# Kernel optimization log

Measured on AMD Instinct MI355X. Metric: run time of the kernel, lower is better.

The kernel has to match this reference:

```python
import jax, jax.numpy as jnp
import numpy as np
import math

N_EMBD = 1024
N_HEAD = 16
D_FF = 4 * N_EMBD
B, T = 4, 2048

def gelu_tanh(x):
    return 0.5 * x * (1.0 + jnp.tanh(jnp.sqrt(2.0 / jnp.pi).astype(x.dtype) * (x + 0.044715 * x ** 3)))

def layernorm(x, g, b, eps=1e-5):
    mu = jnp.mean(x, axis=-1, keepdims=True)
    var = jnp.var(x, axis=-1, keepdims=True)
    return (x - mu) * jax.lax.rsqrt(var + eps) * g + b

def setup_inputs() -> dict:
    key = jax.random.key(0)
    ks = jax.random.split(key, 12)
    s = lambda fan_in: 1.0 / np.sqrt(fan_in)
    return {
        "x": jax.random.normal(ks[0], (B, T, N_EMBD), jnp.float32),
        "ln1_g": jnp.ones((N_EMBD,), jnp.float32),
        "ln1_b": jnp.zeros((N_EMBD,), jnp.float32),
        "w_attn": jax.random.normal(ks[1], (N_EMBD, 3 * N_EMBD), jnp.float32) * s(N_EMBD),
        "b_attn": jnp.zeros((3 * N_EMBD,), jnp.float32),
        "w_proj": jax.random.normal(ks[2], (N_EMBD, N_EMBD), jnp.float32) * s(N_EMBD),
        "b_proj": jnp.zeros((N_EMBD,), jnp.float32),
        "ln2_g": jnp.ones((N_EMBD,), jnp.float32),
        "ln2_b": jnp.zeros((N_EMBD,), jnp.float32),
        "w_fc": jax.random.normal(ks[3], (N_EMBD, D_FF), jnp.float32) * s(N_EMBD),
        "b_fc": jnp.zeros((D_FF,), jnp.float32),
        "w_fc2": jax.random.normal(ks[4], (D_FF, N_EMBD), jnp.float32) * s(D_FF),
        "b_fc2": jnp.zeros((N_EMBD,), jnp.float32),
    }

def reference(x, ln1_g, ln1_b, w_attn, b_attn, w_proj, b_proj,
              ln2_g, ln2_b, w_fc, b_fc, w_fc2, b_fc2):
    Bn, Tn, C = x.shape
    hs = C // N_HEAD
    # --- attention ---
    h = layernorm(x, ln1_g, ln1_b)
    qkv = h @ w_attn + b_attn  # [B,T,3C]
    q, k, v = jnp.split(qkv, 3, axis=-1)
    q = q.reshape(Bn, Tn, N_HEAD, hs).transpose(0, 2, 1, 3)
    k = k.reshape(Bn, Tn, N_HEAD, hs).transpose(0, 2, 1, 3)
    v = v.reshape(Bn, Tn, N_HEAD, hs).transpose(0, 2, 1, 3)
    att = jnp.einsum('bhqd,bhkd->bhqk', q, k) * (hs ** -0.5)
    mask = jnp.tril(jnp.ones((Tn, Tn), bool))
    att = jnp.where(mask, att, -jnp.inf)
    att = jax.nn.softmax(att, axis=-1)
    y = jnp.einsum('bhqk,bhkd->bhqd', att, v)
    y = y.transpose(0, 2, 1, 3).reshape(Bn, Tn, C)
    x = x + (y @ w_proj + b_proj)
    # --- MLP ---
    h2 = layernorm(x, ln2_g, ln2_b)
    h2 = gelu_tanh(h2 @ w_fc + b_fc)
    x = x + (h2 @ w_fc2 + b_fc2)
    return x
```

## Files before the change

### kernel.cpp

```cpp
#include <hip/hip_runtime.h>
#include <hip/hip_bf16.h>

#define B_ 4
#define T_ 2048
#define C_ 1024
#define NH_ 16
#define FF_ 4096
#define NT_ (B_*T_)

typedef short bf16x8 __attribute__((ext_vector_type(8)));
typedef float f32x4 __attribute__((ext_vector_type(4)));

#define LDS_AS(p) ((__attribute__((address_space(3))) uint32_t*)(p))
#define GLB_AS(p) ((const __attribute__((address_space(1))) uint32_t*)(p))

__device__ __forceinline__ float bf2f(__hip_bfloat16 v){ return __bfloat162float(v); }
__device__ __forceinline__ __hip_bfloat16 f2bf(float f){ return __float2bfloat16(f); }

__device__ __forceinline__ f32x4 mfma16(bf16x8 a, bf16x8 b, f32x4 c){
  return __builtin_amdgcn_mfma_f32_16x16x32_bf16(a, b, c, 0, 0, 0);
}

__global__ __launch_bounds__(256) void transpose_bf16(const float* __restrict__ in,
                                                      __hip_bfloat16* __restrict__ out,
                                                      int K, int N) {
  __shared__ float tile[32][33];
  const int n0 = blockIdx.x * 32, k0 = blockIdx.y * 32;
  const int x = threadIdx.x & 31, y = threadIdx.x >> 5;
  #pragma unroll
  for (int i = 0; i < 4; i++)
    tile[y + 8*i][x] = in[(size_t)(k0 + y + 8*i) * N + n0 + x];
  __syncthreads();
  #pragma unroll
  for (int i = 0; i < 4; i++)
    out[(size_t)(n0 + y + 8*i) * K + k0 + x] = f2bf(tile[x][y + 8*i]);
}

__global__ __launch_bounds__(256) void ln_bf16(const float* __restrict__ x,
                                               const float* __restrict__ g,
                                               const float* __restrict__ b,
                                               __hip_bfloat16* __restrict__ out) {
  const int row = blockIdx.x;
  const int tid = threadIdx.x;
  float4 v = ((const float4*)(x + (size_t)row * C_))[tid];
  float s  = v.x + v.y + v.z + v.w;
  float s2 = v.x*v.x + v.y*v.y + v.z*v.z + v.w*v.w;
  #pragma unroll
  for (int off = 32; off > 0; off >>= 1) {
    s  += __shfl_down(s,  off, 64);
    s2 += __shfl_down(s2, off, 64);
  }
  __shared__ float red[8];
  const int w = tid >> 6, l = tid & 63;
  if (l == 0) { red[w] = s; red[4 + w] = s2; }
  __syncthreads();
  s  = red[0] + red[1] + red[2] + red[3];
  s2 = red[4] + red[5] + red[6] + red[7];
  const float mu   = s * (1.0f / C_);
  const float var  = s2 * (1.0f / C_) - mu * mu;
  const float rstd = rsqrtf(var + 1e-5f);
  float4 gv = ((const float4*)g)[tid];
  float4 bv = ((const float4*)b)[tid];
  ushort4 o;
  __hip_bfloat16 t;
  t = f2bf((v.x - mu) * rstd * gv.x + bv.x); o.x = *(unsigned short*)&t;
  t = f2bf((v.y - mu) * rstd * gv.y + bv.y); o.y = *(unsigned short*)&t;
  t = f2bf((v.z - mu) * rstd * gv.z + bv.z); o.z = *(unsigned short*)&t;
  t = f2bf((v.w - mu) * rstd * gv.w + bv.w); o.w = *(unsigned short*)&t;
  ((ushort4*)out)[(size_t)row * (C_/4) + tid] = o;
}

template <int MODE>
__global__ __launch_bounds__(256) void gemm_bt(const __hip_bfloat16* __restrict__ A,
                                               const __hip_bfloat16* __restrict__ BT,
                                               const float* __restrict__ bias,
                                               const float* __restrict__ resid,
                                               void* __restrict__ outp,
                                               void* __restrict__ outp2,
                                               int N, int K) {
  __shared__ __hip_bfloat16 Als[128 * 64];
  __shared__ __hip_bfloat16 Bls[128 * 64];
  const int tid = threadIdx.x;
  const int w = tid >> 6, l = tid & 63;
  const int tile_n = blockIdx.x * 128;
  const int tile_m = blockIdx.y * 128;
  const int wm = (w >> 1) * 64, wn = (w & 1) * 64;

  f32x4 acc[4][4] = {};

  const int lrow8 = l >> 3;
  const int gchunk = (l & 7) ^ lrow8;
  const int m_ = (l & 15);
  const int q_ = (l >> 4);

  for (int k0 = 0; k0 < K; k0 += 64) {
    #pragma unroll
    for (int jj = 0; jj < 2; jj++) {
      const int r0 = w*16 + 8*jj + lrow8;
      __builtin_amdgcn_global_load_lds(GLB_AS(A  + (size_t)(tile_m + r0) * K + k0 + gchunk*8),
                                       LDS_AS(&Als[(w*16 + 8*jj) * 64]), 16, 0, 0);
      __builtin_amdgcn_global_load_lds(GLB_AS(A  + (size_t)(tile_m + 64 + r0) * K + k0 + gchunk*8),
                                       LDS_AS(&Als[(64 + w*16 + 8*jj) * 64]), 16, 0, 0);
      __builtin_amdgcn_global_load_lds(GLB_AS(BT + (size_t)(tile_n + r0) * K + k0 + gchunk*8),
                                       LDS_AS(&Bls[(w*16 + 8*jj) * 64]), 16, 0, 0);
      __builtin_amdgcn_global_load_lds(GLB_AS(BT + (size_t)(tile_n + 64 + r0) * K + k0 + gchunk*8),
                                       LDS_AS(&Bls[(64 + w*16 + 8*jj) * 64]), 16, 0, 0);
    }
    __syncthreads();
    bf16x8 af[2][4], bfr[2][4];
    #pragma unroll
    for (int c = 0; c < 2; c++) {
      #pragma unroll
      for (int mi = 0; mi < 4; mi++) {
        const int row = wm + mi*16 + m_;
        af[c][mi] = *(const bf16x8*)&Als[row * 64 + (((c*4 + q_) ^ (row & 7)) * 8)];
      }
      #pragma unroll
      for (int ni = 0; ni < 4; ni++) {
        const int row = wn + ni*16 + m_;
        bfr[c][ni] = *(const bf16x8*)&Bls[row * 64 + (((c*4 + q_) ^ (row & 7)) * 8)];
      }
    }
    #pragma unroll
    for (int c = 0; c < 2; c++)
      #pragma unroll
      for (int mi = 0; mi < 4; mi++)
        #pragma unroll
        for (int ni = 0; ni < 4; ni++)
          acc[mi][ni] = mfma16(af[c][mi], bfr[c][ni], acc[mi][ni]);
    __syncthreads();
  }

  const int r0 = tile_m + wm + q_ * 4;
  const int c0 = tile_n + wn + m_;
  #pragma unroll
  for (int mi = 0; mi < 4; mi++) {
    #pragma unroll
    for (int r = 0; r < 4; r++) {
      const int row = r0 + mi * 16 + r;
      #pragma unroll
      for (int ni = 0; ni < 4; ni++) {
        const int col = c0 + ni * 16;
        float v = acc[mi][ni][r] + bias[col];
        if (MODE == 0) {
          if (tile_n < 2 * C_) {
            ((__hip_bfloat16*)outp)[(size_t)row * (2*C_) + col] = f2bf(v);
          } else {
            const int dg = col - 2 * C_;
            ((__hip_bfloat16*)outp2)[((size_t)((row >> 11) * 1024 + dg)) * T_ + (row & 2047)] = f2bf(v);
          }
        } else if (MODE == 1 || MODE == 3) {
          ((float*)outp)[(size_t)row * N + col] = resid[(size_t)row * N + col] + v;
        } else {
          const float u = 0.7978845608028654f * (v + 0.044715f * v * v * v);
          const float e = __expf(2.0f * u);
          ((__hip_bfloat16*)outp)[(size_t)row * N + col] = f2bf(v * (1.0f - 1.0f / (e + 1.0f)));
        }
      }
    }
  }
}

__global__ __launch_bounds__(256, 2) void flash_attn(const __hip_bfloat16* __restrict__ qk,
                                                     const __hip_bfloat16* __restrict__ vT,
                                                     __hip_bfloat16* __restrict__ y) {
  const int id  = blockIdx.x;
  const int xcd = id & 7;
  const int jj  = id >> 3;
  const int bh  = xcd * 8 + (jj >> 3);
  const int p   = jj & 7;
  const int b   = bh >> 4, h = bh & 15;
  const int tid = threadIdx.x, w = tid >> 6, l = tid & 63;
  const int m_ = l & 15, q_ = l >> 4;

  __shared__ __hip_bfloat16 Pls[128 * 76];

  const size_t kgbase = (size_t)b * T_ * (2*C_) + C_ + h*64;
  const size_t vgbase = (size_t)bh * 64 * T_;

#define LOAD_KV(bkX, bvX, kt_) do {                                                   \
    _Pragma("unroll")                                                                 \
    for (int ni = 0; ni < 4; ni++) {                                                  \
      const __hip_bfloat16* kp = qk + kgbase + (size_t)((kt_)*64 + ni*16 + m_)*(2*C_);\
      union { uint4 u; bf16x8 f; } t0, t1;                                            \
      t0.u = *(const uint4*)(kp + q_*8);                                              \
      t1.u = *(const uint4*)(kp + 32 + q_*8);                                         \
      bkX[ni][0] = t0.f; bkX[ni][1] = t1.f;                                           \
    }                                                                                 \
    _Pragma("unroll")                                                                 \
    for (int ni = 0; ni < 4; ni++) {                                                  \
      const __hip_bfloat16* vp = vT + vgbase + (size_t)(ni*16 + m_)*T_ + (kt_)*64;    \
      union { uint4 u; bf16x8 f; } t2, t3;                                            \
      t2.u = *(const uint4*)(vp + q_*8);                                              \
      t3.u = *(const uint4*)(vp + 32 + q_*8);                                         \
      bvX[ni][0] = t2.f; bvX[ni][1] = t3.f;                                           \
    }                                                                                 \
  } while (0)

#define COMPUTE(bkX, bvX, kt_) do {                                                   \
    f32x4 s[2][4];                                                                    \
    _Pragma("unroll")                                                                 \
    for (int ni = 0; ni < 4; ni++)                                                    \
      _Pragma("unroll")                                                               \
      for (int mf = 0; mf < 2; mf++) {                                                \
        f32x4 z = {};                                                                 \
        z = mfma16(aq[mf][0], bkX[ni][0], z);                                         \
        s[mf][ni] = mfma16(aq[mf][1], bkX[ni][1], z);                                 \
      }                                                                               \
    if ((kt_) >= 2*qt) {                                                              \
      _Pragma("unroll")                                                               \
      for (int mf = 0; mf < 2; mf++) {                                                \
        const int qrow = q0 + w*32 + mf*16 + q_*4;                                    \
        _Pragma("unroll")                                                             \
        for (int ni = 0; ni < 4; ni++) {                                              \
          const int kcol = (kt_)*64 + ni*16 + m_;                                     \
          _Pragma("unroll")                                                           \
          for (int r = 0; r < 4; r++)                                                 \
            if (kcol > qrow + r) s[mf][ni][r] = -1e30f;                               \
        }                                                                             \
      }                                                                               \
    }                                                                                 \
    _Pragma("unroll")                                                                 \
    for (int mf = 0; mf < 2; mf++) {                                                  \
      _Pragma("unroll")                                                               \
      for (int ni = 0; ni < 4; ni++)                                                  \
        _Pragma("unroll")                                                             \
        for (int r = 0; r < 4; r++)                                                   \
          s[mf][ni][r] = exp2f(s[mf][ni][r]);                                         \
      _Pragma("unroll")                                                               \
      for (int r = 0; r < 4; r++)                                                     \
        lsum[mf][r] += (s[mf][0][r] + s[mf][1][r]) + (s[mf][2][r] + s[mf][3][r]);     \
      _Pragma("unroll")                                                               \
      for (int ni = 0; ni < 4; ni++)                                                  \
        _Pragma("unroll")                                                             \
        for (int r = 0; r < 4; r++)                                                   \
          Pls[(w*32 + mf*16 + q_*4 + r) * 76 + ni*16 + m_] = f2bf(s[mf][ni][r]);      \
    }                                                                                 \
    bf16x8 ap[2][2];                                                                  \
    _Pragma("unroll")                                                                 \
    for (int mf = 0; mf < 2; mf++) {                                                  \
      ap[mf][0] = *(const bf16x8*)&Pls[(w*32 + mf*16 + m_) * 76 + q_*8];              \
      ap[mf][1] = *(const bf16x8*)&Pls[(w*32 + mf*16 + m_) * 76 + 32 + q_*8];         \
    }                                                                                 \
    _Pragma("unroll")                                                                 \
    for (int ni = 0; ni < 4; ni++)                                                    \
      _Pragma("unroll")                                                               \
      for (int mf = 0; mf < 2; mf++) {                                                \
        accO[mf][ni] = mfma16(ap[mf][0], bvX[ni][0], accO[mf][ni]);                   \
        accO[mf][ni] = mfma16(ap[mf][1], bvX[ni][1], accO[mf][ni]);                   \
      }                                                                               \
  } while (0)

  #pragma unroll 1
  for (int ui = 0; ui < 2; ui++) {
    const int qt = ui ? (15 - p) : p;
    const int q0 = qt * 128;

    bf16x8 aq[2][2];
    {
      const float qscale = 0.125f * 1.44269504088896f;
      #pragma unroll
      for (int mf = 0; mf < 2; mf++) {
        const size_t qbase = ((size_t)b * T_ + q0 + w*32 + mf*16 + m_) * (2*C_) + h*64;
        #pragma unroll
        for (int kh = 0; kh < 2; kh++) {
          union { uint4 u; __hip_bfloat16 h8[8]; } t;
          t.u = *(const uint4*)&qk[qbase + kh*32 + q_*8];
          __hip_bfloat16 a[8];
          #pragma unroll
          for (int jx = 0; jx < 8; jx++) a[jx] = f2bf(bf2f(t.h8[jx]) * qscale);
          aq[mf][kh] = *(const bf16x8*)a;
        }
      }
    }

    f32x4 accO[2][4] = {};
    float lsum[2][4] = {{0.f,0.f,0.f,0.f},{0.f,0.f,0.f,0.f}};
    const int ktmax = 2*qt + 1;

    bf16x8 bkA[4][2], bvA[4][2], bkB[4][2], bvB[4][2];
    LOAD_KV(bkA, bvA, 0);
    for (int kt = 0; kt <= ktmax; kt += 2) {
      LOAD_KV(bkB, bvB, kt + 1);
      COMPUTE(bkA, bvA, kt);
      if (kt + 2 <= ktmax) LOAD_KV(bkA, bvA, kt + 2);
      COMPUTE(bkB, bvB, kt + 1);
    }

    #pragma unroll
    for (int mf = 0; mf < 2; mf++)
      #pragma unroll
      for (int r = 0; r < 4; r++) {
        #pragma unroll
        for (int d = 1; d < 16; d <<= 1)
          lsum[mf][r] += __shfl_xor(lsum[mf][r], d, 64);
      }

    const size_t ybase = ((size_t)b * T_ + q0) * C_ + h*64;
    #pragma unroll
    for (int mf = 0; mf < 2; mf++) {
      #pragma unroll
      for (int r = 0; r < 4; r++) {
        const int row = w*32 + mf*16 + q_*4 + r;
        const float linv = 1.0f / lsum[mf][r];
        #pragma unroll
        for (int ni = 0; ni < 4; ni++)
          y[ybase + (size_t)row * C_ + ni*16 + m_] = f2bf(accO[mf][ni][r] * linv);
      }
    }
  }
#undef LOAD_KV
#undef COMPUTE
}

extern "C" void kernel_launch(void* const* d_in, const int* in_sizes, int n_in,
                              void* d_out, int out_size, void* d_ws, size_t ws_size,
                              hipStream_t stream) {
  const float* x      = (const float*)d_in[0];
  const float* ln1_g  = (const float*)d_in[1];
  const float* ln1_b  = (const float*)d_in[2];
  const float* w_attn = (const float*)d_in[3];
  const float* b_attn = (const float*)d_in[4];
  const float* w_proj = (const float*)d_in[5];
  const float* b_proj = (const float*)d_in[6];
  const float* ln2_g  = (const float*)d_in[7];
  const float* ln2_b  = (const float*)d_in[8];
  const float* w_fc   = (const float*)d_in[9];
  const float* b_fc   = (const float*)d_in[10];
  const float* w_fc2  = (const float*)d_in[11];
  const float* b_fc2  = (const float*)d_in[12];
  float* out = (float*)d_out;

  char* ws = (char*)d_ws;
  const size_t MB = 1024 * 1024;
  __hip_bfloat16* h      = (__hip_bfloat16*)(ws);
  __hip_bfloat16* qk     = (__hip_bfloat16*)(ws + 16*MB);
  __hip_bfloat16* vT     = (__hip_bfloat16*)(ws + 48*MB);
  __hip_bfloat16* y      = (__hip_bfloat16*)(ws + 64*MB);
  float*          x2     = (float*)        (ws + 80*MB);
  __hip_bfloat16* h2     = (__hip_bfloat16*)(ws + 64*MB);
  __hip_bfloat16* gbuf   = (__hip_bfloat16*)(ws);
  __hip_bfloat16* wattnT = (__hip_bfloat16*)(ws + 112*MB);
  __hip_bfloat16* wprojT = (__hip_bfloat16*)(ws + 118*MB);
  __hip_bfloat16* wfcT   = (__hip_bfloat16*)(ws + 120*MB);
  __hip_bfloat16* wfc2T  = (__hip_bfloat16*)(ws + 128*MB);

  transpose_bf16<<<dim3(3*C_/32, C_/32), 256, 0, stream>>>(w_attn, wattnT, C_, 3*C_);
  transpose_bf16<<<dim3(C_/32,  C_/32), 256, 0, stream>>>(w_proj, wprojT, C_, C_);
  transpose_bf16<<<dim3(FF_/32, C_/32), 256, 0, stream>>>(w_fc,   wfcT,   C_, FF_);
  transpose_bf16<<<dim3(C_/32, FF_/32), 256, 0, stream>>>(w_fc2,  wfc2T,  FF_, C_);

  ln_bf16<<<NT_, 256, 0, stream>>>(x, ln1_g, ln1_b, h);
  gemm_bt<0><<<dim3(3*C_/128, NT_/128), 256, 0, stream>>>(h, wattnT, b_attn, nullptr, qk, vT, 3*C_, C_);
  flash_attn<<<dim3(512), 256, 0, stream>>>(qk, vT, y);
  gemm_bt<1><<<dim3(C_/128, NT_/128), 256, 0, stream>>>(y, wprojT, b_proj, x, x2, nullptr, C_, C_);
  ln_bf16<<<NT_, 256, 0, stream>>>(x2, ln2_g, ln2_b, h2);
  gemm_bt<2><<<dim3(FF_/128, NT_/128), 256, 0, stream>>>(h2, wfcT, b_fc, nullptr, gbuf, nullptr, FF_, C_);
  gemm_bt<3><<<dim3(C_/128, NT_/128), 256, 0, stream>>>(gbuf, wfc2T, b_fc2, x2, out, nullptr, C_, FF_);
}
```

Baseline: 624.7 us.

## Split flash attention query tiles in half and double block count

Each attention block now handles a 64-row query half-tile instead of 128 rows, and the grid doubles to 1024 blocks with launch bounds raised to 4 blocks per CU. The LDS buffer and register footprint shrink, and the manual double-buffered K/V prefetch is replaced by a simple single-buffered loop that also skips the extra masked tile for the first half. The aim is more occupancy and finer causal work balance. The cost is that each K/V tile is loaded by twice as many blocks, and the software prefetch overlap is lost.

```diff
diff --git a/kernel.cpp b/kernel.cpp
--- a/kernel.cpp
+++ b/kernel.cpp
@@ -161,156 +161,129 @@
   }
 }
 
-__global__ __launch_bounds__(256, 2) void flash_attn(const __hip_bfloat16* __restrict__ qk,
+__global__ __launch_bounds__(256, 4) void flash_attn(const __hip_bfloat16* __restrict__ qk,
                                                      const __hip_bfloat16* __restrict__ vT,
                                                      __hip_bfloat16* __restrict__ y) {
   const int id  = blockIdx.x;
   const int xcd = id & 7;
   const int jj  = id >> 3;
-  const int bh  = xcd * 8 + (jj >> 3);
-  const int p   = jj & 7;
+  const int bh  = xcd * 8 + (jj >> 4);
+  const int p   = (jj >> 1) & 7;
+  const int half= jj & 1;
   const int b   = bh >> 4, h = bh & 15;
   const int tid = threadIdx.x, w = tid >> 6, l = tid & 63;
   const int m_ = l & 15, q_ = l >> 4;
 
-  __shared__ __hip_bfloat16 Pls[128 * 76];
+  __shared__ __hip_bfloat16 Pls[64 * 76];
 
   const size_t kgbase = (size_t)b * T_ * (2*C_) + C_ + h*64;
   const size_t vgbase = (size_t)bh * 64 * T_;
-
-#define LOAD_KV(bkX, bvX, kt_) do {                                                   \
-    _Pragma("unroll")                                                                 \
-    for (int ni = 0; ni < 4; ni++) {                                                  \
-      const __hip_bfloat16* kp = qk + kgbase + (size_t)((kt_)*64 + ni*16 + m_)*(2*C_);\
-      union { uint4 u; bf16x8 f; } t0, t1;                                            \
-      t0.u = *(const uint4*)(kp + q_*8);                                              \
-      t1.u = *(const uint4*)(kp + 32 + q_*8);                                         \
-      bkX[ni][0] = t0.f; bkX[ni][1] = t1.f;                                           \
-    }                                                                                 \
-    _Pragma("unroll")                                                                 \
-    for (int ni = 0; ni < 4; ni++) {                                                  \
-      const __hip_bfloat16* vp = vT + vgbase + (size_t)(ni*16 + m_)*T_ + (kt_)*64;    \
-      union { uint4 u; bf16x8 f; } t2, t3;                                            \
-      t2.u = *(const uint4*)(vp + q_*8);                                              \
-      t3.u = *(const uint4*)(vp + 32 + q_*8);                                         \
-      bvX[ni][0] = t2.f; bvX[ni][1] = t3.f;                                           \
-    }                                                                                 \
-  } while (0)
-
-#define COMPUTE(bkX, bvX, kt_) do {                                                   \
-    f32x4 s[2][4];                                                                    \
-    _Pragma("unroll")                                                                 \
-    for (int ni = 0; ni < 4; ni++)                                                    \
-      _Pragma("unroll")                                                               \
-      for (int mf = 0; mf < 2; mf++) {                                                \
-        f32x4 z = {};                                                                 \
-        z = mfma16(aq[mf][0], bkX[ni][0], z);                                         \
-        s[mf][ni] = mfma16(aq[mf][1], bkX[ni][1], z);                                 \
-      }                                                                               \
-    if ((kt_) >= 2*qt) {                                                              \
-      _Pragma("unroll")                                                               \
-      for (int mf = 0; mf < 2; mf++) {                                                \
-        const int qrow = q0 + w*32 + mf*16 + q_*4;                                    \
-        _Pragma("unroll")                                                             \
-        for (int ni = 0; ni < 4; ni++) {                                              \
-          const int kcol = (kt_)*64 + ni*16 + m_;                                     \
-          _Pragma("unroll")                                                           \
-          for (int r = 0; r < 4; r++)                                                 \
-            if (kcol > qrow + r) s[mf][ni][r] = -1e30f;                               \
-        }                                                                             \
-      }                                                                               \
-    }                                                                                 \
-    _Pragma("unroll")                                                                 \
-    for (int mf = 0; mf < 2; mf++) {                                                  \
-      _Pragma("unroll")                                                               \
-      for (int ni = 0; ni < 4; ni++)                                                  \
-        _Pragma("unroll")                                                             \
-        for (int r = 0; r < 4; r++)                                                   \
-          s[mf][ni][r] = exp2f(s[mf][ni][r]);                                         \
-      _Pragma("unroll")                                                               \
-      for (int r = 0; r < 4; r++)                                                     \
-        lsum[mf][r] += (s[mf][0][r] + s[mf][1][r]) + (s[mf][2][r] + s[mf][3][r]);     \
-      _Pragma("unroll")                                                               \
-      for (int ni = 0; ni < 4; ni++)                                                  \
-        _Pragma("unroll")                                                             \
-        for (int r = 0; r < 4; r++)                                                   \
-          Pls[(w*32 + mf*16 + q_*4 + r) * 76 + ni*16 + m_] = f2bf(s[mf][ni][r]);      \
-    }                                                                                 \
-    bf16x8 ap[2][2];                                                                  \
-    _Pragma("unroll")                                                                 \
-    for (int mf = 0; mf < 2; mf++) {                                                  \
-      ap[mf][0] = *(const bf16x8*)&Pls[(w*32 + mf*16 + m_) * 76 + q_*8];              \
-      ap[mf][1] = *(const bf16x8*)&Pls[(w*32 + mf*16 + m_) * 76 + 32 + q_*8];         \
-    }                                                                                 \
-    _Pragma("unroll")                                                                 \
-    for (int ni = 0; ni < 4; ni++)                                                    \
-      _Pragma("unroll")                                                               \
-      for (int mf = 0; mf < 2; mf++) {                                                \
-        accO[mf][ni] = mfma16(ap[mf][0], bvX[ni][0], accO[mf][ni]);                   \
-        accO[mf][ni] = mfma16(ap[mf][1], bvX[ni][1], accO[mf][ni]);                   \
-      }                                                                               \
-  } while (0)
 
   #pragma unroll 1
   for (int ui = 0; ui < 2; ui++) {
     const int qt = ui ? (15 - p) : p;
-    const int q0 = qt * 128;
-
-    bf16x8 aq[2][2];
+    const int q0 = qt * 128 + half * 64;
+
+    bf16x8 aq[2];
     {
       const float qscale = 0.125f * 1.44269504088896f;
-      #pragma unroll
-      for (int mf = 0; mf < 2; mf++) {
-        const size_t qbase = ((size_t)b * T_ + q0 + w*32 + mf*16 + m_) * (2*C_) + h*64;
-        #pragma unroll
-        for (int kh = 0; kh < 2; kh++) {
-          union { uint4 u; __hip_bfloat16 h8[8]; } t;
-          t.u = *(const uint4*)&qk[qbase + kh*32 + q_*8];
-          __hip_bfloat16 a[8];
+      const size_t qbase = ((size_t)b * T_ + q0 + w*16 + m_) * (2*C_) + h*64;
+      #pragma unroll
+      for (int kh = 0; kh < 2; kh++) {
+        union { uint4 u; __hip_bfloat16 h8[8]; } t;
+        t.u = *(const uint4*)&qk[qbase + kh*32 + q_*8];
+        __hip_bfloat16 a[8];
+        #pragma unroll
+        for (int jx = 0; jx < 8; jx++) a[jx] = f2bf(bf2f(t.h8[jx]) * qscale);
+        aq[kh] = *(const bf16x8*)a;
+      }
+    }
+
+    f32x4 accO[4] = {};
+    float lsum[4] = {0.f, 0.f, 0.f, 0.f};
+    const int ktlast = 2*qt + half;
+
+    #pragma unroll 1
+    for (int kt = 0; kt <= ktlast; kt++) {
+      bf16x8 bk[4][2], bv[4][2];
+      #pragma unroll
+      for (int ni = 0; ni < 4; ni++) {
+        const __hip_bfloat16* kp = qk + kgbase + (size_t)(kt*64 + ni*16 + m_)*(2*C_);
+        union { uint4 u; bf16x8 f; } t0, t1;
+        t0.u = *(const uint4*)(kp + q_*8);
+        t1.u = *(const uint4*)(kp + 32 + q_*8);
+        bk[ni][0] = t0.f; bk[ni][1] = t1.f;
+      }
+      #pragma unroll
+      for (int ni = 0; ni < 4; ni++) {
+        const __hip_bfloat16* vp = vT + vgbase + (size_t)(ni*16 + m_)*T_ + kt*64;
+        union { uint4 u; bf16x8 f; } t2, t3;
+        t2.u = *(const uint4*)(vp + q_*8);
+        t3.u = *(const uint4*)(vp + 32 + q_*8);
+        bv[ni][0] = t2.f; bv[ni][1] = t3.f;
+      }
+
+      f32x4 s[4];
+      #pragma unroll
+      for (int ni = 0; ni < 4; ni++) {
+        f32x4 z = {};
+        z = mfma16(aq[0], bk[ni][0], z);
+        s[ni] = mfma16(aq[1], bk[ni][1], z);
+      }
+
+      if (kt == ktlast) {
+        const int qrow = q0 + w*16 + q_*4;
+        #pragma unroll
+        for (int ni = 0; ni < 4; ni++) {
+          const int kcol = kt*64 + ni*16 + m_;
           #pragma unroll
-          for (int jx = 0; jx < 8; jx++) a[jx] = f2bf(bf2f(t.h8[jx]) * qscale);
-          aq[mf][kh] = *(const bf16x8*)a;
+          for (int r = 0; r < 4; r++)
+            if (kcol > qrow + r) s[ni][r] = -1e30f;
         }
       }
-    }
-
-    f32x4 accO[2][4] = {};
-    float lsum[2][4] = {{0.f,0.f,0.f,0.f},{0.f,0.f,0.f,0.f}};
-    const int ktmax = 2*qt + 1;
-
-    bf16x8 bkA[4][2], bvA[4][2], bkB[4][2], bvB[4][2];
-    LOAD_KV(bkA, bvA, 0);
-    for (int kt = 0; kt <= ktmax; kt += 2) {
-      LOAD_KV(bkB, bvB, kt + 1);
-      COMPUTE(bkA, bvA, kt);
-      if (kt + 2 <= ktmax) LOAD_KV(bkA, bvA, kt + 2);
-      COMPUTE(bkB, bvB, kt + 1);
-    }
-
-    #pragma unroll
-    for (int mf = 0; mf < 2; mf++)
-      #pragma unroll
-      for (int r = 0; r < 4; r++) {
-        #pragma unroll
-        for (int d = 1; d < 16; d <<= 1)
-          lsum[mf][r] += __shfl_xor(lsum[mf][r], d, 64);
-      }
+
+      #pragma unroll
+      for (int ni = 0; ni < 4; ni++)
+        #pragma unroll
+        for (int r = 0; r < 4; r++)
+          s[ni][r] = exp2f(s[ni][r]);
+      #pragma unroll
+      for (int r = 0; r < 4; r++)
+        lsum[r] += (s[0][r] + s[1][r]) + (s[2][r] + s[3][r]);
+      #pragma unroll
+      for (int ni = 0; ni < 4; ni++)
+        #pragma unroll
+        for (int r = 0; r < 4; r++)
+          Pls[(w*16 + q_*4 + r) * 76 + ni*16 + m_] = f2bf(s[ni][r]);
+
+      bf16x8 ap[2];
+      ap[0] = *(const bf16x8*)&Pls[(w*16 + m_) * 76 + q_*8];
+      ap[1] = *(const bf16x8*)&Pls[(w*16 + m_) * 76 + 32 + q_*8];
+
+      #pragma unroll
+      for (int ni = 0; ni < 4; ni++) {
+        accO[ni] = mfma16(ap[0], bv[ni][0], accO[ni]);
+        accO[ni] = mfma16(ap[1], bv[ni][1], accO[ni]);
+      }
+    }
+
+    #pragma unroll
+    for (int r = 0; r < 4; r++) {
+      #pragma unroll
+      for (int d = 1; d < 16; d <<= 1)
+        lsum[r] += __shfl_xor(lsum[r], d, 64);
+    }
 
     const size_t ybase = ((size_t)b * T_ + q0) * C_ + h*64;
     #pragma unroll
-    for (int mf = 0; mf < 2; mf++) {
-      #pragma unroll
-      for (int r = 0; r < 4; r++) {
-        const int row = w*32 + mf*16 + q_*4 + r;
-        const float linv = 1.0f / lsum[mf][r];
-        #pragma unroll
-        for (int ni = 0; ni < 4; ni++)
-          y[ybase + (size_t)row * C_ + ni*16 + m_] = f2bf(accO[mf][ni][r] * linv);
-      }
+    for (int r = 0; r < 4; r++) {
+      const int row = w*16 + q_*4 + r;
+      const float linv = 1.0f / lsum[r];
+      #pragma unroll
+      for (int ni = 0; ni < 4; ni++)
+        y[ybase + (size_t)row * C_ + ni*16 + m_] = f2bf(accO[ni][r] * linv);
     }
   }
-#undef LOAD_KV
-#undef COMPUTE
 }
 
 extern "C" void kernel_launch(void* const* d_in, const int* in_sizes, int n_in,
@@ -352,7 +325,7 @@
 
   ln_bf16<<<NT_, 256, 0, stream>>>(x, ln1_g, ln1_b, h);
   gemm_bt<0><<<dim3(3*C_/128, NT_/128), 256, 0, stream>>>(h, wattnT, b_attn, nullptr, qk, vT, 3*C_, C_);
-  flash_attn<<<dim3(512), 256, 0, stream>>>(qk, vT, y);
+  flash_attn<<<dim3(1024), 256, 0, stream>>>(qk, vT, y);
   gemm_bt<1><<<dim3(C_/128, NT_/128), 256, 0, stream>>>(y, wprojT, b_proj, x, x2, nullptr, C_, C_);
   ln_bf16<<<NT_, 256, 0, stream>>>(x2, ln2_g, ln2_b, h2);
   gemm_bt<2><<<dim3(FF_/128, NT_/128), 256, 0, stream>>>(h2, wfcT, b_fc, nullptr, gbuf, nullptr, FF_, C_);
```

Result: slower. 710.1 us (+13.7%).
